# Performance work log

Hardware: AMD Instinct MI355X
Metric: run time of the kernel (lower is better)

Reference implementation:

```python
import jax, jax.numpy as jnp
import numpy as np

HEADS = 16

def setup_inputs() -> dict:
    key = jax.random.key(0)
    ks = jax.random.split(key, 6)
    b, n, d, k = 4, 4096, 1024, 256
    return {
        "x": jax.random.normal(ks[0], (b, n, d), dtype=jnp.float32),
        "Wq": jax.random.normal(ks[1], (d, d), dtype=jnp.float32) * 0.02,
        "Wk": jax.random.normal(ks[2], (d, d), dtype=jnp.float32) * 0.02,
        "Wv": jax.random.normal(ks[3], (d, d), dtype=jnp.float32) * 0.02,
        "proj_k": jax.random.normal(ks[4], (n, k), dtype=jnp.float32) * 0.02,
        "proj_v": jax.random.normal(ks[5], (n, k), dtype=jnp.float32) * 0.02,
    }

def reference(x, Wq, Wk, Wv, proj_k, proj_v):
    b, n, d = x.shape
    h = HEADS
    dh = d // h
    k = proj_k.shape[1]
    # Q/K/V projections (no bias)
    q = jnp.einsum('bnd,de->bne', x, Wq)          # [b,n,d]
    keys = jnp.einsum('bnd,de->bne', x, Wk)       # [b,n,d]
    vals = jnp.einsum('bnd,de->bne', x, Wv)       # [b,n,d]
    # low-rank sequence projection: n -> k
    keys = jnp.einsum('bnd,nk->bkd', keys, proj_k)   # [b,k,d]
    vals = jnp.einsum('bnd,nk->bkd', vals, proj_v)   # [b,k,d]
    # split heads
    q = q.reshape(b, n, h, dh).transpose(0, 2, 1, 3)      # [b,h,n,dh]
    keys = keys.reshape(b, k, h, dh).transpose(0, 2, 1, 3)  # [b,h,k,dh]
    vals = vals.reshape(b, k, h, dh).transpose(0, 2, 1, 3)  # [b,h,k,dh]
    # attention over reduced k dim (NOTE: module applies no 1/sqrt(dh) scale)
    dots = jnp.einsum('bhnd,bhkd->bhnk', q, keys)
    attn = jax.nn.softmax(dots, axis=-1)
    out = jnp.einsum('bhnk,bhkd->bhnd', attn, vals)
    return out.transpose(0, 2, 1, 3).reshape(b, n, d)
```

## Files before the change

### kernel.cpp

```cpp
#include <hip/hip_runtime.h>


typedef __fp16 f16x8 __attribute__((ext_vector_type(8)));
typedef __fp16 f16x2 __attribute__((ext_vector_type(2)));
typedef float fl4 __attribute__((ext_vector_type(4)));
typedef float f32x4 __attribute__((ext_vector_type(4)));
typedef unsigned int u32x2 __attribute__((ext_vector_type(2)));
typedef unsigned int u32x4 __attribute__((ext_vector_type(4)));

#define MFMA16(a, b, c) __builtin_amdgcn_mfma_f32_16x16x32_f16((a), (b), (c), 0, 0, 0)

__device__ __forceinline__ unsigned int pk2u(float a, float b) {
  f16x2 p = __builtin_amdgcn_cvt_pkrtz(a, b);
  return __builtin_bit_cast(unsigned int, p);
}

__device__ __forceinline__ f16x8 pk8(fl4 a, fl4 b) {
  f16x2 p0 = __builtin_amdgcn_cvt_pkrtz(a[0], a[1]);
  f16x2 p1 = __builtin_amdgcn_cvt_pkrtz(a[2], a[3]);
  f16x2 p2 = __builtin_amdgcn_cvt_pkrtz(b[0], b[1]);
  f16x2 p3 = __builtin_amdgcn_cvt_pkrtz(b[2], b[3]);
  f16x8 r;
  r[0] = p0[0]; r[1] = p0[1]; r[2] = p1[0]; r[3] = p1[1];
  r[4] = p2[0]; r[5] = p2[1]; r[6] = p3[0]; r[7] = p3[1];
  return r;
}

__device__ __forceinline__ void gload_lds16(const __fp16* g, void* lds_base) {
  __builtin_amdgcn_global_load_lds(
      (const __attribute__((address_space(1))) void*)g,
      (__attribute__((address_space(3))) void*)lds_base, 16, 0, 0);
}

__device__ __forceinline__ f16x8 rd128(const __fp16* base, int row, int ch) {
  return *(const f16x8*)((const char*)base + row * 128 +
                         ((ch ^ (row & 7)) * 16));
}

__device__ __forceinline__ void tr_cvt_body(
    float* tile, const float* in, __fp16* out, int R, int C, int bx, int by) {
  const int t = threadIdx.x;
  const int c0 = bx * 32, r0 = by * 32;
  {
    const int r = t >> 3, cg = (t & 7) * 4;
    fl4 v = *(const fl4*)(in + (size_t)(r0 + r) * C + c0 + cg);
    tile[r * 33 + cg] = v[0]; tile[r * 33 + cg + 1] = v[1];
    tile[r * 33 + cg + 2] = v[2]; tile[r * 33 + cg + 3] = v[3];
  }
  __syncthreads();
  {
    const int cc = t >> 3, rg = (t & 7) * 4;
    u32x2 p;
    p[0] = pk2u(tile[(rg + 0) * 33 + cc], tile[(rg + 1) * 33 + cc]);
    p[1] = pk2u(tile[(rg + 2) * 33 + cc], tile[(rg + 3) * 33 + cc]);
    *(u32x2*)(out + (size_t)(c0 + cc) * R + r0 + rg) = p;
  }
}

__global__ __launch_bounds__(256) void prep(
    const float* __restrict__ X, __fp16* __restrict__ Xf,
    __fp16* __restrict__ XT,
    const float* __restrict__ Wq, const float* __restrict__ Wk,
    const float* __restrict__ Wv, __fp16* __restrict__ WqT,
    __fp16* __restrict__ WkT, __fp16* __restrict__ WvT,
    const float* __restrict__ pk, const float* __restrict__ pv,
    __fp16* __restrict__ pkT, __fp16* __restrict__ pvT) {
  __shared__ float tile[32 * 65];
  const int id = blockIdx.x;
  const int t = threadIdx.x;
  if (id < 8192) {
    const int n0 = (id & 127) * 32, d0 = ((id >> 7) & 15) * 64, b = id >> 11;
    const float* src = X + ((size_t)b * 4096 + n0) * 1024 + d0;
    {
      const int r = t >> 3, cg = (t & 7) * 8;
      fl4 v0 = *(const fl4*)(src + (size_t)r * 1024 + cg);
      fl4 v1 = *(const fl4*)(src + (size_t)r * 1024 + cg + 4);
      *(f16x8*)(Xf + ((size_t)b * 4096 + n0 + r) * 1024 + d0 + cg) = pk8(v0, v1);
#pragma unroll
      for (int j = 0; j < 4; ++j) {
        tile[r * 65 + cg + j] = v0[j];
        tile[r * 65 + cg + 4 + j] = v1[j];
      }
    }
    __syncthreads();
    {
      const int d = t >> 2, ng = (t & 3) * 8;
      fl4 a, c;
#pragma unroll
      for (int j = 0; j < 4; ++j) {
        a[j] = tile[(ng + j) * 65 + d];
        c[j] = tile[(ng + 4 + j) * 65 + d];
      }
      *(f16x8*)(XT + ((size_t)b * 1024 + d0 + d) * 4096 + n0 + ng) = pk8(a, c);
    }
  } else if (id < 11264) {
    const int idx = id - 8192;
    const int z = idx >> 10;
    const float* in = (z == 0) ? Wq : (z == 1) ? Wk : Wv;
    __fp16* out = (z == 0) ? WqT : (z == 1) ? WkT : WvT;
    tr_cvt_body(tile, in, out, 1024, 1024, idx & 31, (idx >> 5) & 31);
  } else {
    const int idx = id - 11264;
    const int z = idx >> 10;
    tr_cvt_body(tile, z ? pv : pk, z ? pvT : pkT, 4096, 256, idx & 7,
                (idx >> 3) & 127);
  }
}

__global__ __launch_bounds__(256) void stage1_partial(
    const __fp16* __restrict__ pkT,
    const __fp16* __restrict__ pvT,
    const __fp16* __restrict__ XT,
    __fp16* __restrict__ Pk,
    __fp16* __restrict__ Pv) {
  __shared__ __fp16 Ak[64 * 64];
  __shared__ __fp16 Av[64 * 64];
  __shared__ __fp16 Bx[64 * 64];
  const int t = threadIdx.x;
  const int lane = t & 63, w = t >> 6;
  const int lr = lane & 15, lg = lane >> 4;
  const int fid = blockIdx.x;
  const int g = fid >> 5, s5 = fid & 31;
  const int kk0 = (s5 >> 3) * 64, p8 = s5 & 7;
  const int pr = g * 8 + p8;
  const int dd0 = (pr & 15) * 64;
  const int z = pr >> 4, b = z & 3, c = z >> 2;
  const int wr = (w >> 1) * 32, wc = (w & 1) * 32;

  f32x4 acck[2][2], accv[2][2];
#pragma unroll
  for (int i = 0; i < 2; ++i)
#pragma unroll
    for (int j = 0; j < 2; ++j) {
      acck[i][j] = (f32x4){0.f, 0.f, 0.f, 0.f};
      accv[i][j] = (f32x4){0.f, 0.f, 0.f, 0.f};
    }

  const int r8 = lane >> 3, c8 = lane & 7;
  const int ssw = ((c8 ^ r8) * 8);
  const __fp16* pkS0 = pkT + (size_t)(kk0 + w * 8 + r8) * 4096 + c * 1024 + ssw;
  const __fp16* pkS1 = pkS0 + (size_t)32 * 4096;
  const __fp16* pvS0 = pvT + (size_t)(kk0 + w * 8 + r8) * 4096 + c * 1024 + ssw;
  const __fp16* pvS1 = pvS0 + (size_t)32 * 4096;
  const __fp16* xS0 =
      XT + ((size_t)b * 1024 + dd0 + w * 8 + r8) * 4096 + c * 1024 + ssw;
  const __fp16* xS1 = xS0 + (size_t)32 * 4096;

  for (int it = 0; it < 16; ++it) {
    const int n0 = it * 64;
    __syncthreads();
    gload_lds16(pkS0 + n0, (char*)Ak + w * 1024);
    gload_lds16(pkS1 + n0, (char*)Ak + 4096 + w * 1024);
    gload_lds16(pvS0 + n0, (char*)Av + w * 1024);
    gload_lds16(pvS1 + n0, (char*)Av + 4096 + w * 1024);
    gload_lds16(xS0 + n0, (char*)Bx + w * 1024);
    gload_lds16(xS1 + n0, (char*)Bx + 4096 + w * 1024);
    __syncthreads();

#pragma unroll
    for (int s = 0; s < 2; ++s) {
      f16x8 ak[2], av[2], bx[2];
#pragma unroll
      for (int i = 0; i < 2; ++i) {
        ak[i] = rd128(Ak, wr + i * 16 + lr, s * 4 + lg);
        av[i] = rd128(Av, wr + i * 16 + lr, s * 4 + lg);
      }
#pragma unroll
      for (int j = 0; j < 2; ++j)
        bx[j] = rd128(Bx, wc + j * 16 + lr, s * 4 + lg);
#pragma unroll
      for (int i = 0; i < 2; ++i)
#pragma unroll
        for (int j = 0; j < 2; ++j) {
          acck[i][j] = MFMA16(ak[i], bx[j], acck[i][j]);
          accv[i][j] = MFMA16(av[i], bx[j], accv[i][j]);
        }
    }
  }

#pragma unroll
  for (int i = 0; i < 2; ++i)
#pragma unroll
    for (int j = 0; j < 2; ++j)
#pragma unroll
      for (int r = 0; r < 4; ++r) {
        const size_t row = (size_t)z * 256 + kk0 + wr + i * 16 + lg * 4 + r;
        const int col = dd0 + wc + j * 16 + lr;
        Pk[row * 1024 + col] = (__fp16)acck[i][j][r];
        Pv[row * 1024 + col] = (__fp16)accv[i][j][r];
      }
}

__global__ __launch_bounds__(256) void stage1_reduce(
    const __fp16* __restrict__ Pk, const __fp16* __restrict__ Pv,
    __fp16* __restrict__ Xk, __fp16* __restrict__ Xv) {
  const size_t idx = ((size_t)blockIdx.x * 256 + threadIdx.x) * 8;
  const int b = (int)(idx >> 18);
  const size_t rem = idx & 0x3FFFFu;
  float sk[8], sv[8];
#pragma unroll
  for (int j = 0; j < 8; ++j) { sk[j] = 0.f; sv[j] = 0.f; }
#pragma unroll
  for (int c = 0; c < 4; ++c) {
    const size_t off = (((size_t)(c * 4 + b)) << 18) + rem;
    f16x8 vk = *(const f16x8*)(Pk + off);
    f16x8 vv = *(const f16x8*)(Pv + off);
#pragma unroll
    for (int j = 0; j < 8; ++j) {
      sk[j] += (float)vk[j];
      sv[j] += (float)vv[j];
    }
  }
  f16x8 ok, ov;
#pragma unroll
  for (int j = 0; j < 8; ++j) {
    ok[j] = (__fp16)sk[j];
    ov[j] = (__fp16)sv[j];
  }
  *(f16x8*)(Xk + idx) = ok;
  *(f16x8*)(Xv + idx) = ov;
}

__global__ __launch_bounds__(256) void bt64z(
    const __fp16* __restrict__ Xk, const __fp16* __restrict__ WkT,
    __fp16* __restrict__ Kp, const __fp16* __restrict__ WvT,
    const __fp16* __restrict__ Xv, __fp16* __restrict__ Vpt) {
  constexpr int E = 1024;
  __shared__ __fp16 As[64 * 64];
  __shared__ __fp16 Bs[64 * 64];
  const int t = threadIdx.x;
  const int lane = t & 63, w = t >> 6;
  const int lr = lane & 15, lg = lane >> 4;
  int id = blockIdx.x;
  const __fp16 *A, *B;
  __fp16* C;
  int i0, j0, ldC;
  if (id < 256) {
    const int x = id & 3, y = (id >> 2) & 15, z = id >> 6;
    A = Xk + (size_t)z * 256 * 1024; B = WkT;
    C = Kp + (size_t)z * 256 * 1024;
    i0 = x * 64; j0 = y * 64; ldC = 1024;
  } else {
    id -= 256;
    const int x = id & 15, y = (id >> 4) & 3, z = id >> 6;
    A = WvT; B = Xv + (size_t)z * 256 * 1024;
    C = Vpt + (size_t)z * 1024 * 256;
    i0 = x * 64; j0 = y * 64; ldC = 256;
  }
  const int wr = (w >> 1) * 32, wc = (w & 1) * 32;

  f32x4 acc[2][2];
#pragma unroll
  for (int i = 0; i < 2; ++i)
#pragma unroll
    for (int j = 0; j < 2; ++j) acc[i][j] = (f32x4){0.f, 0.f, 0.f, 0.f};

  const int r8 = lane >> 3, c8 = lane & 7;
  const int ssw = ((c8 ^ r8) * 8);
  const __fp16* aS0 = A + (size_t)(i0 + w * 8 + r8) * E + ssw;
  const __fp16* aS1 = aS0 + (size_t)32 * E;
  const __fp16* bS0 = B + (size_t)(j0 + w * 8 + r8) * E + ssw;
  const __fp16* bS1 = bS0 + (size_t)32 * E;

  for (int it = 0; it < 16; ++it) {
    const int e0 = it * 64;
    __syncthreads();
    gload_lds16(aS0 + e0, (char*)As + w * 1024);
    gload_lds16(aS1 + e0, (char*)As + 4096 + w * 1024);
    gload_lds16(bS0 + e0, (char*)Bs + w * 1024);
    gload_lds16(bS1 + e0, (char*)Bs + 4096 + w * 1024);
    __syncthreads();

#pragma unroll
    for (int s = 0; s < 2; ++s) {
      f16x8 af[2], bf[2];
#pragma unroll
      for (int i = 0; i < 2; ++i)
        af[i] = rd128(As, wr + i * 16 + lr, s * 4 + lg);
#pragma unroll
      for (int j = 0; j < 2; ++j)
        bf[j] = rd128(Bs, wc + j * 16 + lr, s * 4 + lg);
#pragma unroll
      for (int i = 0; i < 2; ++i)
#pragma unroll
        for (int j = 0; j < 2; ++j)
          acc[i][j] = MFMA16(af[i], bf[j], acc[i][j]);
    }
  }

#pragma unroll
  for (int i = 0; i < 2; ++i)
#pragma unroll
    for (int j = 0; j < 2; ++j)
#pragma unroll
      for (int r = 0; r < 4; ++r) {
        const int row = i0 + wr + i * 16 + lg * 4 + r;
        const int col = j0 + wc + j * 16 + lr;
        C[(size_t)row * ldC + col] = (__fp16)acc[i][j][r];
      }
}

__global__ __launch_bounds__(512) void gemm_q(
    const __fp16* __restrict__ Xf,
    const __fp16* __restrict__ WT,
    __fp16* __restrict__ Q) {
  constexpr int K = 1024, N = 1024;
  __shared__ __fp16 Xs[256 * 64];
  __shared__ __fp16 Ws[128 * 64];
  const int t = threadIdx.x;
  const int lane = t & 63, w = t >> 6;
  const int lr = lane & 15, lg = lane >> 4;
  const int fid = blockIdx.x;
  const int m0 = (fid & 63) * 256;
  const int n0 = (fid >> 6) * 128;
  const int wr = (w & 3) * 64, wc = (w >> 2) * 64;

  f32x4 acc[4][4];
#pragma unroll
  for (int i = 0; i < 4; ++i)
#pragma unroll
    for (int j = 0; j < 4; ++j) acc[i][j] = (f32x4){0.f, 0.f, 0.f, 0.f};

  const int r8 = lane >> 3, c8 = lane & 7;
  const int ssw = ((c8 ^ r8) * 8);
  const __fp16* xS = Xf + (size_t)(m0 + w * 8 + r8) * K + ssw;
  const __fp16* wS = WT + (size_t)(n0 + w * 8 + r8) * K + ssw;

  for (int it = 0; it < 16; ++it) {
    const int k0 = it * 64;
    __syncthreads();
#pragma unroll
    for (int i = 0; i < 4; ++i)
      gload_lds16(xS + (size_t)i * 64 * K + k0, (char*)Xs + i * 8192 + w * 1024);
#pragma unroll
    for (int i = 0; i < 2; ++i)
      gload_lds16(wS + (size_t)i * 64 * K + k0, (char*)Ws + i * 8192 + w * 1024);
    __syncthreads();

#pragma unroll
    for (int s = 0; s < 2; ++s) {
      f16x8 af[4], bf[4];
#pragma unroll
      for (int i = 0; i < 4; ++i)
        af[i] = rd128(Xs, wr + i * 16 + lr, s * 4 + lg);
#pragma unroll
      for (int j = 0; j < 4; ++j)
        bf[j] = rd128(Ws, wc + j * 16 + lr, s * 4 + lg);
#pragma unroll
      for (int i = 0; i < 4; ++i)
#pragma unroll
        for (int j = 0; j < 4; ++j)
          acc[i][j] = MFMA16(af[i], bf[j], acc[i][j]);
    }
  }

#pragma unroll
  for (int i = 0; i < 4; ++i)
#pragma unroll
    for (int j = 0; j < 4; ++j)
#pragma unroll
      for (int r = 0; r < 4; ++r) {
        const int row = m0 + wr + i * 16 + lg * 4 + r;
        const int col = n0 + wc + j * 16 + lr;
        Q[(size_t)row * N + col] = (__fp16)acc[i][j][r];
      }
}

__global__ __launch_bounds__(256) void attn_k(
    const __fp16* __restrict__ Q,
    const __fp16* __restrict__ Kp,
    const __fp16* __restrict__ Vpt,
    float* __restrict__ O) {
  __shared__ __fp16 KV[256 * 64];
  const int t = threadIdx.x;
  const int lane = t & 63, w = t >> 6;
  const int lr = lane & 15, lg = lane >> 4;
  const int bh = blockIdx.x >> 5, rb = blockIdx.x & 31;
  const int b = bh >> 4, h = bh & 15;
  const int m0 = rb * 128 + w * 32;

  const __fp16* Kph = Kp + (size_t)b * 256 * 1024 + h * 64;
  const __fp16* Vph = Vpt + ((size_t)b * 1024 + h * 64) * 256;
  const __fp16* Qh = Q + ((size_t)(b * 4096 + m0)) * 1024 + h * 64;

#pragma unroll
  for (int i = 0; i < 8; ++i) {
    const int kr = (i * 4 + w) * 8 + (lane >> 3);
    gload_lds16(Kph + (size_t)kr * 1024 + (((lane & 7) ^ (kr & 7)) * 8),
                (char*)KV + (i * 4 + w) * 1024);
  }

  f16x8 aq[2][2];
#pragma unroll
  for (int mi = 0; mi < 2; ++mi)
#pragma unroll
    for (int s = 0; s < 2; ++s)
      aq[mi][s] =
          *(const f16x8*)(Qh + (size_t)(mi * 16 + lr) * 1024 + s * 32 + lg * 8);

  __syncthreads();

  f32x4 dots[2][16];
#pragma unroll
  for (int mi = 0; mi < 2; ++mi)
#pragma unroll
    for (int jt = 0; jt < 16; ++jt) dots[mi][jt] = (f32x4){0.f, 0.f, 0.f, 0.f};
#pragma unroll
  for (int jt = 0; jt < 16; ++jt) {
    const int r = jt * 16 + lr;
    f16x8 k0 = *(const f16x8*)((const char*)KV + r * 128 + ((lg ^ (r & 7)) * 16));
    f16x8 k1 =
        *(const f16x8*)((const char*)KV + r * 128 + (((4 + lg) ^ (r & 7)) * 16));
    dots[0][jt] = MFMA16(k0, aq[0][0], dots[0][jt]);
    dots[0][jt] = MFMA16(k1, aq[0][1], dots[0][jt]);
    dots[1][jt] = MFMA16(k0, aq[1][0], dots[1][jt]);
    dots[1][jt] = MFMA16(k1, aq[1][1], dots[1][jt]);
  }

  unsigned cpk[2][16][2];
  float smv[2];
#pragma unroll
  for (int mi = 0; mi < 2; ++mi) {
    float mx = -1e30f;
#pragma unroll
    for (int jt = 0; jt < 16; ++jt)
#pragma unroll
      for (int r = 0; r < 4; ++r) mx = fmaxf(mx, dots[mi][jt][r]);
    mx = fmaxf(mx, __shfl_xor(mx, 16, 64));
    mx = fmaxf(mx, __shfl_xor(mx, 32, 64));
    float sm = 0.f;
#pragma unroll
    for (int jt = 0; jt < 16; ++jt) {
#pragma unroll
      for (int r = 0; r < 4; ++r) {
        float p = __expf(dots[mi][jt][r] - mx);
        dots[mi][jt][r] = p;
        sm += p;
      }
      cpk[mi][jt][0] = pk2u(dots[mi][jt][0], dots[mi][jt][1]);
      cpk[mi][jt][1] = pk2u(dots[mi][jt][2], dots[mi][jt][3]);
    }
    sm += __shfl_xor(sm, 16, 64);
    sm += __shfl_xor(sm, 32, 64);
    smv[mi] = sm;
  }

  __syncthreads();

#pragma unroll
  for (int i = 0; i < 8; ++i) {
    const int dd = (i * 4 + w) * 2 + (lane >> 5);
    gload_lds16(Vph + (size_t)dd * 256 + (((lane & 31) ^ (dd & 7)) * 8),
                (char*)KV + (i * 4 + w) * 1024);
  }
  __syncthreads();

#pragma unroll
  for (int mi = 0; mi < 2; ++mi) {
    f32x4 o[4];
#pragma unroll
    for (int j = 0; j < 4; ++j) o[j] = (f32x4){0.f, 0.f, 0.f, 0.f};
#pragma unroll
    for (int ks = 0; ks < 8; ++ks) {
      u32x4 wds;
#pragma unroll
      for (int m = 0; m < 4; ++m) {
        const int addr = ((((lane & 16) >> 3) + (m >> 1)) * 16 + lr) * 4;
        const int a0 = __builtin_amdgcn_ds_bpermute(
            addr, (int)cpk[mi][ks * 2][m & 1]);
        const int a1 = __builtin_amdgcn_ds_bpermute(
            addr, (int)cpk[mi][ks * 2 + 1][m & 1]);
        wds[m] = (unsigned)((lg >> 1) ? a1 : a0);
      }
      f16x8 pa = __builtin_bit_cast(f16x8, wds);
#pragma unroll
      for (int jt2 = 0; jt2 < 4; ++jt2) {
        const int dd = jt2 * 16 + lr;
        f16x8 bv = *(const f16x8*)((const char*)KV + dd * 512 +
                                   (((ks * 4 + lg) ^ (dd & 7)) * 16));
        o[jt2] = MFMA16(pa, bv, o[jt2]);
      }
    }

    float rs[4];
#pragma unroll
    for (int r = 0; r < 4; ++r)
      rs[r] = 1.f / __shfl(smv[mi], (lane & 48) + lg * 4 + r, 64);
#pragma unroll
    for (int jt2 = 0; jt2 < 4; ++jt2)
#pragma unroll
      for (int r = 0; r < 4; ++r) {
        const size_t row = (size_t)(b * 4096 + m0 + mi * 16 + lg * 4 + r);
        O[row * 1024 + h * 64 + jt2 * 16 + lr] = o[jt2][r] * rs[r];
      }
  }
}

extern "C" void kernel_launch(void* const* d_in, const int* in_sizes, int n_in,
                              void* d_out, int out_size, void* d_ws, size_t ws_size,
                              hipStream_t stream) {
  (void)in_sizes; (void)n_in; (void)out_size; (void)ws_size;
  const float* x  = (const float*)d_in[0];
  const float* Wq = (const float*)d_in[1];
  const float* Wk = (const float*)d_in[2];
  const float* Wv = (const float*)d_in[3];
  const float* pk = (const float*)d_in[4];
  const float* pv = (const float*)d_in[5];
  float* out = (float*)d_out;

  __fp16* Qh  = (__fp16*)d_ws;
  __fp16* WqT = Qh  + (size_t)16384 * 1024;
  __fp16* WkT = WqT + (size_t)1024 * 1024;
  __fp16* WvT = WkT + (size_t)1024 * 1024;
  __fp16* pkT = WvT + (size_t)1024 * 1024;
  __fp16* pvT = pkT + (size_t)256 * 4096;
  __fp16* Xk  = pvT + (size_t)256 * 4096;
  __fp16* Xv  = Xk  + (size_t)4 * 256 * 1024;
  __fp16* Kp  = Xv  + (size_t)4 * 256 * 1024;
  __fp16* Vpt = Kp  + (size_t)4 * 256 * 1024;
  __fp16* Pk16 = (__fp16*)d_ws;
  __fp16* Pv16 = Pk16 + (size_t)16 * 256 * 1024;
  __fp16* Xf16 = (__fp16*)d_out;
  __fp16* XT   = Xf16 + (size_t)4 * 4096 * 1024;

  const dim3 bb(256);

  prep<<<dim3(13312), bb, 0, stream>>>(x, Xf16, XT, Wq, Wk, Wv, WqT, WkT, WvT,
                                       pk, pv, pkT, pvT);

  stage1_partial<<<dim3(1024), bb, 0, stream>>>(pkT, pvT, XT, Pk16, Pv16);
  stage1_reduce<<<dim3(512), bb, 0, stream>>>(Pk16, Pv16, Xk, Xv);

  bt64z<<<dim3(512), bb, 0, stream>>>(Xk, WkT, Kp, WvT, Xv, Vpt);

  gemm_q<<<dim3(512), dim3(512), 0, stream>>>(Xf16, WqT, Qh);

  attn_k<<<dim3(2048), bb, 0, stream>>>(Qh, Kp, Vpt, out);
}
```

Baseline: 155.8 us.

## Merge Q projection GEMM and stage1 partial into one launch

After: 157.6 us. No clear change (+1.2%).

```diff
diff --git a/kernel.cpp b/kernel.cpp
--- a/kernel.cpp
+++ b/kernel.cpp
@@ -189,6 +189,222 @@
         Pk[row * 1024 + col] = (__fp16)acck[i][j][r];
         Pv[row * 1024 + col] = (__fp16)accv[i][j][r];
       }
+}
+
+__global__ __launch_bounds__(512) void gemm_q(
+    const __fp16* __restrict__ Xf,
+    const __fp16* __restrict__ WT,
+    __fp16* __restrict__ Q) {
+  constexpr int K = 1024, N = 1024;
+  __shared__ __fp16 Xs[256 * 64];
+  __shared__ __fp16 Ws[128 * 64];
+  const int t = threadIdx.x;
+  const int lane = t & 63, w = t >> 6;
+  const int lr = lane & 15, lg = lane >> 4;
+  const int fid = blockIdx.x;
+  const int m0 = (fid & 63) * 256;
+  const int n0 = (fid >> 6) * 128;
+  const int wr = (w & 3) * 64, wc = (w >> 2) * 64;
+
+  f32x4 acc[4][4];
+#pragma unroll
+  for (int i = 0; i < 4; ++i)
+#pragma unroll
+    for (int j = 0; j < 4; ++j) acc[i][j] = (f32x4){0.f, 0.f, 0.f, 0.f};
+
+  const int r8 = lane >> 3, c8 = lane & 7;
+  const int ssw = ((c8 ^ r8) * 8);
+  const __fp16* xS = Xf + (size_t)(m0 + w * 8 + r8) * K + ssw;
+  const __fp16* wS = WT + (size_t)(n0 + w * 8 + r8) * K + ssw;
+
+  for (int it = 0; it < 16; ++it) {
+    const int k0 = it * 64;
+    __syncthreads();
+#pragma unroll
+    for (int i = 0; i < 4; ++i)
+      gload_lds16(xS + (size_t)i * 64 * K + k0, (char*)Xs + i * 8192 + w * 1024);
+#pragma unroll
+    for (int i = 0; i < 2; ++i)
+      gload_lds16(wS + (size_t)i * 64 * K + k0, (char*)Ws + i * 8192 + w * 1024);
+    __syncthreads();
+
+#pragma unroll
+    for (int s = 0; s < 2; ++s) {
+      f16x8 af[4], bf[4];
+#pragma unroll
+      for (int i = 0; i < 4; ++i)
+        af[i] = rd128(Xs, wr + i * 16 + lr, s * 4 + lg);
+#pragma unroll
+      for (int j = 0; j < 4; ++j)
+        bf[j] = rd128(Ws, wc + j * 16 + lr, s * 4 + lg);
+#pragma unroll
+      for (int i = 0; i < 4; ++i)
+#pragma unroll
+        for (int j = 0; j < 4; ++j)
+          acc[i][j] = MFMA16(af[i], bf[j], acc[i][j]);
+    }
+  }
+
+#pragma unroll
+  for (int i = 0; i < 4; ++i)
+#pragma unroll
+    for (int j = 0; j < 4; ++j)
+#pragma unroll
+      for (int r = 0; r < 4; ++r) {
+        const int row = m0 + wr + i * 16 + lg * 4 + r;
+        const int col = n0 + wc + j * 16 + lr;
+        Q[(size_t)row * N + col] = (__fp16)acc[i][j][r];
+      }
+}
+
+__global__ __launch_bounds__(512) void midphase(
+    const __fp16* __restrict__ Xf, const __fp16* __restrict__ WqT,
+    __fp16* __restrict__ Q,
+    const __fp16* __restrict__ pkT, const __fp16* __restrict__ pvT,
+    const __fp16* __restrict__ XT,
+    __fp16* __restrict__ Pk, __fp16* __restrict__ Pv) {
+  __shared__ __fp16 smem[24576];
+  const int id = blockIdx.x;
+  const int t = threadIdx.x;
+  const int lane = t & 63, w = t >> 6;
+  const int lr = lane & 15, lg = lane >> 4;
+  const int r8 = lane >> 3, c8 = lane & 7;
+  const int ssw = ((c8 ^ r8) * 8);
+
+  if (id < 512) {
+    constexpr int K = 1024, N = 1024;
+    __fp16* Xs = smem;
+    __fp16* Ws = smem + 16384;
+    const int m0 = (id & 63) * 256;
+    const int n0 = (id >> 6) * 128;
+    const int wr = (w & 3) * 64, wc = (w >> 2) * 64;
+
+    f32x4 acc[4][4];
+#pragma unroll
+    for (int i = 0; i < 4; ++i)
+#pragma unroll
+      for (int j = 0; j < 4; ++j) acc[i][j] = (f32x4){0.f, 0.f, 0.f, 0.f};
+
+    const __fp16* xS = Xf + (size_t)(m0 + w * 8 + r8) * K + ssw;
+    const __fp16* wS = WqT + (size_t)(n0 + w * 8 + r8) * K + ssw;
+
+    for (int it = 0; it < 16; ++it) {
+      const int k0 = it * 64;
+      __syncthreads();
+#pragma unroll
+      for (int i = 0; i < 4; ++i)
+        gload_lds16(xS + (size_t)i * 64 * K + k0, (char*)Xs + i * 8192 + w * 1024);
+#pragma unroll
+      for (int i = 0; i < 2; ++i)
+        gload_lds16(wS + (size_t)i * 64 * K + k0, (char*)Ws + i * 8192 + w * 1024);
+      __syncthreads();
+
+#pragma unroll
+      for (int s = 0; s < 2; ++s) {
+        f16x8 af[4], bf[4];
+#pragma unroll
+        for (int i = 0; i < 4; ++i)
+          af[i] = rd128(Xs, wr + i * 16 + lr, s * 4 + lg);
+#pragma unroll
+        for (int j = 0; j < 4; ++j)
+          bf[j] = rd128(Ws, wc + j * 16 + lr, s * 4 + lg);
+#pragma unroll
+        for (int i = 0; i < 4; ++i)
+#pragma unroll
+          for (int j = 0; j < 4; ++j)
+            acc[i][j] = MFMA16(af[i], bf[j], acc[i][j]);
+      }
+    }
+
+#pragma unroll
+    for (int i = 0; i < 4; ++i)
+#pragma unroll
+      for (int j = 0; j < 4; ++j)
+#pragma unroll
+        for (int r = 0; r < 4; ++r) {
+          const int row = m0 + wr + i * 16 + lg * 4 + r;
+          const int col = n0 + wc + j * 16 + lr;
+          Q[(size_t)row * N + col] = (__fp16)acc[i][j][r];
+        }
+  } else {
+    __fp16* Ak = smem;
+    __fp16* Av = smem + 4096;
+    __fp16* Bx = smem + 8192;
+    const int fid = id - 512;
+    const int g = fid >> 5, s5 = fid & 31;
+    const int kk0 = (s5 >> 3) * 64, p8 = s5 & 7;
+    const int pr = g * 8 + p8;
+    const int dd0 = (pr & 15) * 64;
+    const int z = pr >> 4, b = z & 3, c = z >> 2;
+    const int wr = (w >> 1) * 32, wc = (w & 1) * 32;
+
+    f32x4 acck[2][2], accv[2][2];
+#pragma unroll
+    for (int i = 0; i < 2; ++i)
+#pragma unroll
+      for (int j = 0; j < 2; ++j) {
+        acck[i][j] = (f32x4){0.f, 0.f, 0.f, 0.f};
+        accv[i][j] = (f32x4){0.f, 0.f, 0.f, 0.f};
+      }
+
+    const __fp16* pkS0 = pkT + (size_t)(kk0 + (w & 3) * 8 + r8) * 4096 + c * 1024 + ssw;
+    const __fp16* pkS1 = pkS0 + (size_t)32 * 4096;
+    const __fp16* pvS0 = pvT + (size_t)(kk0 + (w & 3) * 8 + r8) * 4096 + c * 1024 + ssw;
+    const __fp16* pvS1 = pvS0 + (size_t)32 * 4096;
+    const __fp16* xS0 =
+        XT + ((size_t)b * 1024 + dd0 + (w & 3) * 8 + r8) * 4096 + c * 1024 + ssw;
+    const __fp16* xS1 = xS0 + (size_t)32 * 4096;
+
+    for (int it = 0; it < 16; ++it) {
+      const int n0 = it * 64;
+      __syncthreads();
+      if (w < 4) {
+        gload_lds16(pkS0 + n0, (char*)Ak + w * 1024);
+        gload_lds16(pkS1 + n0, (char*)Ak + 4096 + w * 1024);
+        gload_lds16(pvS0 + n0, (char*)Av + w * 1024);
+        gload_lds16(pvS1 + n0, (char*)Av + 4096 + w * 1024);
+        gload_lds16(xS0 + n0, (char*)Bx + w * 1024);
+        gload_lds16(xS1 + n0, (char*)Bx + 4096 + w * 1024);
+      }
+      __syncthreads();
+
+      if (w < 4) {
+#pragma unroll
+        for (int s = 0; s < 2; ++s) {
+          f16x8 ak[2], av[2], bx[2];
+#pragma unroll
+          for (int i = 0; i < 2; ++i) {
+            ak[i] = rd128(Ak, wr + i * 16 + lr, s * 4 + lg);
+            av[i] = rd128(Av, wr + i * 16 + lr, s * 4 + lg);
+          }
+#pragma unroll
+          for (int j = 0; j < 2; ++j)
+            bx[j] = rd128(Bx, wc + j * 16 + lr, s * 4 + lg);
+#pragma unroll
+          for (int i = 0; i < 2; ++i)
+#pragma unroll
+            for (int j = 0; j < 2; ++j) {
+              acck[i][j] = MFMA16(ak[i], bx[j], acck[i][j]);
+              accv[i][j] = MFMA16(av[i], bx[j], accv[i][j]);
+            }
+        }
+      }
+    }
+
+    if (w < 4) {
+#pragma unroll
+      for (int i = 0; i < 2; ++i)
+#pragma unroll
+        for (int j = 0; j < 2; ++j)
+#pragma unroll
+          for (int r = 0; r < 4; ++r) {
+            const size_t row = (size_t)z * 256 + kk0 + wr + i * 16 + lg * 4 + r;
+            const int col = dd0 + wc + j * 16 + lr;
+            Pk[row * 1024 + col] = (__fp16)acck[i][j][r];
+            Pv[row * 1024 + col] = (__fp16)accv[i][j][r];
+          }
+    }
+  }
 }
 
 __global__ __launch_bounds__(256) void stage1_reduce(
@@ -300,72 +516,6 @@
       }
 }
 
-__global__ __launch_bounds__(512) void gemm_q(
-    const __fp16* __restrict__ Xf,
-    const __fp16* __restrict__ WT,
-    __fp16* __restrict__ Q) {
-  constexpr int K = 1024, N = 1024;
-  __shared__ __fp16 Xs[256 * 64];
-  __shared__ __fp16 Ws[128 * 64];
-  const int t = threadIdx.x;
-  const int lane = t & 63, w = t >> 6;
-  const int lr = lane & 15, lg = lane >> 4;
-  const int fid = blockIdx.x;
-  const int m0 = (fid & 63) * 256;
-  const int n0 = (fid >> 6) * 128;
-  const int wr = (w & 3) * 64, wc = (w >> 2) * 64;
-
-  f32x4 acc[4][4];
-#pragma unroll
-  for (int i = 0; i < 4; ++i)
-#pragma unroll
-    for (int j = 0; j < 4; ++j) acc[i][j] = (f32x4){0.f, 0.f, 0.f, 0.f};
-
-  const int r8 = lane >> 3, c8 = lane & 7;
-  const int ssw = ((c8 ^ r8) * 8);
-  const __fp16* xS = Xf + (size_t)(m0 + w * 8 + r8) * K + ssw;
-  const __fp16* wS = WT + (size_t)(n0 + w * 8 + r8) * K + ssw;
-
-  for (int it = 0; it < 16; ++it) {
-    const int k0 = it * 64;
-    __syncthreads();
-#pragma unroll
-    for (int i = 0; i < 4; ++i)
-      gload_lds16(xS + (size_t)i * 64 * K + k0, (char*)Xs + i * 8192 + w * 1024);
-#pragma unroll
-    for (int i = 0; i < 2; ++i)
-      gload_lds16(wS + (size_t)i * 64 * K + k0, (char*)Ws + i * 8192 + w * 1024);
-    __syncthreads();
-
-#pragma unroll
-    for (int s = 0; s < 2; ++s) {
-      f16x8 af[4], bf[4];
-#pragma unroll
-      for (int i = 0; i < 4; ++i)
-        af[i] = rd128(Xs, wr + i * 16 + lr, s * 4 + lg);
-#pragma unroll
-      for (int j = 0; j < 4; ++j)
-        bf[j] = rd128(Ws, wc + j * 16 + lr, s * 4 + lg);
-#pragma unroll
-      for (int i = 0; i < 4; ++i)
-#pragma unroll
-        for (int j = 0; j < 4; ++j)
-          acc[i][j] = MFMA16(af[i], bf[j], acc[i][j]);
-    }
-  }
-
-#pragma unroll
-  for (int i = 0; i < 4; ++i)
-#pragma unroll
-    for (int j = 0; j < 4; ++j)
-#pragma unroll
-      for (int r = 0; r < 4; ++r) {
-        const int row = m0 + wr + i * 16 + lg * 4 + r;
-        const int col = n0 + wc + j * 16 + lr;
-        Q[(size_t)row * N + col] = (__fp16)acc[i][j][r];
-      }
-}
-
 __global__ __launch_bounds__(256) void attn_k(
     const __fp16* __restrict__ Q,
     const __fp16* __restrict__ Kp,
@@ -499,7 +649,7 @@
 extern "C" void kernel_launch(void* const* d_in, const int* in_sizes, int n_in,
                               void* d_out, int out_size, void* d_ws, size_t ws_size,
                               hipStream_t stream) {
-  (void)in_sizes; (void)n_in; (void)out_size; (void)ws_size;
+  (void)in_sizes; (void)n_in; (void)out_size;
   const float* x  = (const float*)d_in[0];
   const float* Wq = (const float*)d_in[1];
   const float* Wk = (const float*)d_in[2];
@@ -518,22 +668,31 @@
   __fp16* Xv  = Xk  + (size_t)4 * 256 * 1024;
   __fp16* Kp  = Xv  + (size_t)4 * 256 * 1024;
   __fp16* Vpt = Kp  + (size_t)4 * 256 * 1024;
-  __fp16* Pk16 = (__fp16*)d_ws;
-  __fp16* Pv16 = Pk16 + (size_t)16 * 256 * 1024;
+  __fp16* wsEnd = Vpt + (size_t)4 * 256 * 1024;
   __fp16* Xf16 = (__fp16*)d_out;
   __fp16* XT   = Xf16 + (size_t)4 * 4096 * 1024;
 
+  const size_t needB = 52428800ULL + 2ULL * 16 * 256 * 1024 * 2;
+  const bool bigWs = (ws_size >= needB);
+  __fp16* Pk16 = bigWs ? wsEnd : (__fp16*)d_ws;
+  __fp16* Pv16 = Pk16 + (size_t)16 * 256 * 1024;
+
   const dim3 bb(256);
 
   prep<<<dim3(13312), bb, 0, stream>>>(x, Xf16, XT, Wq, Wk, Wv, WqT, WkT, WvT,
                                        pk, pv, pkT, pvT);
 
-  stage1_partial<<<dim3(1024), bb, 0, stream>>>(pkT, pvT, XT, Pk16, Pv16);
-  stage1_reduce<<<dim3(512), bb, 0, stream>>>(Pk16, Pv16, Xk, Xv);
-
-  bt64z<<<dim3(512), bb, 0, stream>>>(Xk, WkT, Kp, WvT, Xv, Vpt);
-
-  gemm_q<<<dim3(512), dim3(512), 0, stream>>>(Xf16, WqT, Qh);
+  if (bigWs) {
+    midphase<<<dim3(1536), dim3(512), 0, stream>>>(Xf16, WqT, Qh, pkT, pvT, XT,
+                                                   Pk16, Pv16);
+    stage1_reduce<<<dim3(512), bb, 0, stream>>>(Pk16, Pv16, Xk, Xv);
+    bt64z<<<dim3(512), bb, 0, stream>>>(Xk, WkT, Kp, WvT, Xv, Vpt);
+  } else {
+    stage1_partial<<<dim3(1024), bb, 0, stream>>>(pkT, pvT, XT, Pk16, Pv16);
+    stage1_reduce<<<dim3(512), bb, 0, stream>>>(Pk16, Pv16, Xk, Xv);
+    bt64z<<<dim3(512), bb, 0, stream>>>(Xk, WkT, Kp, WvT, Xv, Vpt);
+    gemm_q<<<dim3(512), dim3(512), 0, stream>>>(Xf16, WqT, Qh);
+  }
 
   attn_k<<<dim3(2048), bb, 0, stream>>>(Qh, Kp, Vpt, out);
 }
```

## Co-schedule Q projection GEMM with stage1 partial reduction in one launch

Applied to the files above, without the earlier changes.

After: 152.1 us, median of 2. 1.02x faster.

```diff
diff --git a/kernel.cpp b/kernel.cpp
--- a/kernel.cpp
+++ b/kernel.cpp
@@ -107,25 +107,18 @@
   }
 }
 
-__global__ __launch_bounds__(256) void stage1_partial(
-    const __fp16* __restrict__ pkT,
-    const __fp16* __restrict__ pvT,
-    const __fp16* __restrict__ XT,
-    __fp16* __restrict__ Pk,
-    __fp16* __restrict__ Pv) {
-  __shared__ __fp16 Ak[64 * 64];
-  __shared__ __fp16 Av[64 * 64];
-  __shared__ __fp16 Bx[64 * 64];
-  const int t = threadIdx.x;
-  const int lane = t & 63, w = t >> 6;
+__device__ __forceinline__ void stage1_tile(
+    const __fp16* __restrict__ pkT, const __fp16* __restrict__ pvT,
+    const __fp16* __restrict__ XT, __fp16* __restrict__ Pk,
+    __fp16* __restrict__ Pv, __fp16* Ak, __fp16* Av, __fp16* Bx,
+    int fid, int ww, int lane) {
   const int lr = lane & 15, lg = lane >> 4;
-  const int fid = blockIdx.x;
   const int g = fid >> 5, s5 = fid & 31;
   const int kk0 = (s5 >> 3) * 64, p8 = s5 & 7;
   const int pr = g * 8 + p8;
   const int dd0 = (pr & 15) * 64;
   const int z = pr >> 4, b = z & 3, c = z >> 2;
-  const int wr = (w >> 1) * 32, wc = (w & 1) * 32;
+  const int wr = (ww >> 1) * 32, wc = (ww & 1) * 32;
 
   f32x4 acck[2][2], accv[2][2];
 #pragma unroll
@@ -138,23 +131,23 @@
 
   const int r8 = lane >> 3, c8 = lane & 7;
   const int ssw = ((c8 ^ r8) * 8);
-  const __fp16* pkS0 = pkT + (size_t)(kk0 + w * 8 + r8) * 4096 + c * 1024 + ssw;
+  const __fp16* pkS0 = pkT + (size_t)(kk0 + ww * 8 + r8) * 4096 + c * 1024 + ssw;
   const __fp16* pkS1 = pkS0 + (size_t)32 * 4096;
-  const __fp16* pvS0 = pvT + (size_t)(kk0 + w * 8 + r8) * 4096 + c * 1024 + ssw;
+  const __fp16* pvS0 = pvT + (size_t)(kk0 + ww * 8 + r8) * 4096 + c * 1024 + ssw;
   const __fp16* pvS1 = pvS0 + (size_t)32 * 4096;
   const __fp16* xS0 =
-      XT + ((size_t)b * 1024 + dd0 + w * 8 + r8) * 4096 + c * 1024 + ssw;
+      XT + ((size_t)b * 1024 + dd0 + ww * 8 + r8) * 4096 + c * 1024 + ssw;
   const __fp16* xS1 = xS0 + (size_t)32 * 4096;
 
   for (int it = 0; it < 16; ++it) {
     const int n0 = it * 64;
     __syncthreads();
-    gload_lds16(pkS0 + n0, (char*)Ak + w * 1024);
-    gload_lds16(pkS1 + n0, (char*)Ak + 4096 + w * 1024);
-    gload_lds16(pvS0 + n0, (char*)Av + w * 1024);
-    gload_lds16(pvS1 + n0, (char*)Av + 4096 + w * 1024);
-    gload_lds16(xS0 + n0, (char*)Bx + w * 1024);
-    gload_lds16(xS1 + n0, (char*)Bx + 4096 + w * 1024);
+    gload_lds16(pkS0 + n0, (char*)Ak + ww * 1024);
+    gload_lds16(pkS1 + n0, (char*)Ak + 4096 + ww * 1024);
+    gload_lds16(pvS0 + n0, (char*)Av + ww * 1024);
+    gload_lds16(pvS1 + n0, (char*)Av + 4096 + ww * 1024);
+    gload_lds16(xS0 + n0, (char*)Bx + ww * 1024);
+    gload_lds16(xS1 + n0, (char*)Bx + 4096 + ww * 1024);
     __syncthreads();
 
 #pragma unroll
@@ -189,6 +182,106 @@
         Pk[row * 1024 + col] = (__fp16)acck[i][j][r];
         Pv[row * 1024 + col] = (__fp16)accv[i][j][r];
       }
+}
+
+__global__ __launch_bounds__(256) void stage1_partial(
+    const __fp16* __restrict__ pkT, const __fp16* __restrict__ pvT,
+    const __fp16* __restrict__ XT, __fp16* __restrict__ Pk,
+    __fp16* __restrict__ Pv) {
+  __shared__ __fp16 smem[12288];
+  const int t = threadIdx.x;
+  stage1_tile(pkT, pvT, XT, Pk, Pv, smem, smem + 4096, smem + 8192,
+              blockIdx.x, t >> 6, t & 63);
+}
+
+__device__ __forceinline__ void gemmq_tile(
+    const __fp16* __restrict__ Xf, const __fp16* __restrict__ WT,
+    __fp16* __restrict__ Q, __fp16* Xs, __fp16* Ws, int fid, int w,
+    int lane) {
+  constexpr int K = 1024, N = 1024;
+  const int lr = lane & 15, lg = lane >> 4;
+  const int m0 = (fid & 63) * 256;
+  const int n0 = (fid >> 6) * 128;
+  const int wr = (w & 3) * 64, wc = (w >> 2) * 64;
+
+  f32x4 acc[4][4];
+#pragma unroll
+  for (int i = 0; i < 4; ++i)
+#pragma unroll
+    for (int j = 0; j < 4; ++j) acc[i][j] = (f32x4){0.f, 0.f, 0.f, 0.f};
+
+  const int r8 = lane >> 3, c8 = lane & 7;
+  const int ssw = ((c8 ^ r8) * 8);
+  const __fp16* xS = Xf + (size_t)(m0 + w * 8 + r8) * K + ssw;
+  const __fp16* wS = WT + (size_t)(n0 + w * 8 + r8) * K + ssw;
+
+  for (int it = 0; it < 16; ++it) {
+    const int k0 = it * 64;
+    __syncthreads();
+#pragma unroll
+    for (int i = 0; i < 4; ++i)
+      gload_lds16(xS + (size_t)i * 64 * K + k0, (char*)Xs + i * 8192 + w * 1024);
+#pragma unroll
+    for (int i = 0; i < 2; ++i)
+      gload_lds16(wS + (size_t)i * 64 * K + k0, (char*)Ws + i * 8192 + w * 1024);
+    __syncthreads();
+
+#pragma unroll
+    for (int s = 0; s < 2; ++s) {
+      f16x8 af[4], bf[4];
+#pragma unroll
+      for (int i = 0; i < 4; ++i)
+        af[i] = rd128(Xs, wr + i * 16 + lr, s * 4 + lg);
+#pragma unroll
+      for (int j = 0; j < 4; ++j)
+        bf[j] = rd128(Ws, wc + j * 16 + lr, s * 4 + lg);
+#pragma unroll
+      for (int i = 0; i < 4; ++i)
+#pragma unroll
+        for (int j = 0; j < 4; ++j)
+          acc[i][j] = MFMA16(af[i], bf[j], acc[i][j]);
+    }
+  }
+
+#pragma unroll
+  for (int i = 0; i < 4; ++i)
+#pragma unroll
+    for (int j = 0; j < 4; ++j)
+#pragma unroll
+      for (int r = 0; r < 4; ++r) {
+        const int row = m0 + wr + i * 16 + lg * 4 + r;
+        const int col = n0 + wc + j * 16 + lr;
+        Q[(size_t)row * N + col] = (__fp16)acc[i][j][r];
+      }
+}
+
+__global__ __launch_bounds__(512) void gemm_q(
+    const __fp16* __restrict__ Xf, const __fp16* __restrict__ WT,
+    __fp16* __restrict__ Q) {
+  __shared__ __fp16 smem[24576];
+  const int t = threadIdx.x;
+  gemmq_tile(Xf, WT, Q, smem, smem + 16384, blockIdx.x, t >> 6, t & 63);
+}
+
+__global__ __launch_bounds__(512) void midphase(
+    const __fp16* __restrict__ Xf, const __fp16* __restrict__ WqT,
+    __fp16* __restrict__ Q,
+    const __fp16* __restrict__ pkT, const __fp16* __restrict__ pvT,
+    const __fp16* __restrict__ XT,
+    __fp16* __restrict__ Pk, __fp16* __restrict__ Pv) {
+  __shared__ __fp16 smem[24576];
+  const int id = blockIdx.x;
+  const int t = threadIdx.x;
+  const int lane = t & 63, w = t >> 6;
+
+  if (id < 512) {
+    gemmq_tile(Xf, WqT, Q, smem, smem + 16384, id, w, lane);
+  } else {
+    const int grp = w >> 2, ww = w & 3;
+    __fp16* base = smem + grp * 12288;
+    stage1_tile(pkT, pvT, XT, Pk, Pv, base, base + 4096, base + 8192,
+                (id - 512) * 2 + grp, ww, lane);
+  }
 }
 
 __global__ __launch_bounds__(256) void stage1_reduce(
@@ -300,72 +393,6 @@
       }
 }
 
-__global__ __launch_bounds__(512) void gemm_q(
-    const __fp16* __restrict__ Xf,
-    const __fp16* __restrict__ WT,
-    __fp16* __restrict__ Q) {
-  constexpr int K = 1024, N = 1024;
-  __shared__ __fp16 Xs[256 * 64];
-  __shared__ __fp16 Ws[128 * 64];
-  const int t = threadIdx.x;
-  const int lane = t & 63, w = t >> 6;
-  const int lr = lane & 15, lg = lane >> 4;
-  const int fid = blockIdx.x;
-  const int m0 = (fid & 63) * 256;
-  const int n0 = (fid >> 6) * 128;
-  const int wr = (w & 3) * 64, wc = (w >> 2) * 64;
-
-  f32x4 acc[4][4];
-#pragma unroll
-  for (int i = 0; i < 4; ++i)
-#pragma unroll
-    for (int j = 0; j < 4; ++j) acc[i][j] = (f32x4){0.f, 0.f, 0.f, 0.f};
-
-  const int r8 = lane >> 3, c8 = lane & 7;
-  const int ssw = ((c8 ^ r8) * 8);
-  const __fp16* xS = Xf + (size_t)(m0 + w * 8 + r8) * K + ssw;
-  const __fp16* wS = WT + (size_t)(n0 + w * 8 + r8) * K + ssw;
-
-  for (int it = 0; it < 16; ++it) {
-    const int k0 = it * 64;
-    __syncthreads();
-#pragma unroll
-    for (int i = 0; i < 4; ++i)
-      gload_lds16(xS + (size_t)i * 64 * K + k0, (char*)Xs + i * 8192 + w * 1024);
-#pragma unroll
-    for (int i = 0; i < 2; ++i)
-      gload_lds16(wS + (size_t)i * 64 * K + k0, (char*)Ws + i * 8192 + w * 1024);
-    __syncthreads();
-
-#pragma unroll
-    for (int s = 0; s < 2; ++s) {
-      f16x8 af[4], bf[4];
-#pragma unroll
-      for (int i = 0; i < 4; ++i)
-        af[i] = rd128(Xs, wr + i * 16 + lr, s * 4 + lg);
-#pragma unroll
-      for (int j = 0; j < 4; ++j)
-        bf[j] = rd128(Ws, wc + j * 16 + lr, s * 4 + lg);
-#pragma unroll
-      for (int i = 0; i < 4; ++i)
-#pragma unroll
-        for (int j = 0; j < 4; ++j)
-          acc[i][j] = MFMA16(af[i], bf[j], acc[i][j]);
-    }
-  }
-
-#pragma unroll
-  for (int i = 0; i < 4; ++i)
-#pragma unroll
-    for (int j = 0; j < 4; ++j)
-#pragma unroll
-      for (int r = 0; r < 4; ++r) {
-        const int row = m0 + wr + i * 16 + lg * 4 + r;
-        const int col = n0 + wc + j * 16 + lr;
-        Q[(size_t)row * N + col] = (__fp16)acc[i][j][r];
-      }
-}
-
 __global__ __launch_bounds__(256) void attn_k(
     const __fp16* __restrict__ Q,
     const __fp16* __restrict__ Kp,
@@ -499,7 +526,7 @@
 extern "C" void kernel_launch(void* const* d_in, const int* in_sizes, int n_in,
                               void* d_out, int out_size, void* d_ws, size_t ws_size,
                               hipStream_t stream) {
-  (void)in_sizes; (void)n_in; (void)out_size; (void)ws_size;
+  (void)in_sizes; (void)n_in; (void)out_size;
   const float* x  = (const float*)d_in[0];
   const float* Wq = (const float*)d_in[1];
   const float* Wk = (const float*)d_in[2];
@@ -518,22 +545,31 @@
   __fp16* Xv  = Xk  + (size_t)4 * 256 * 1024;
   __fp16* Kp  = Xv  + (size_t)4 * 256 * 1024;
   __fp16* Vpt = Kp  + (size_t)4 * 256 * 1024;
-  __fp16* Pk16 = (__fp16*)d_ws;
-  __fp16* Pv16 = Pk16 + (size_t)16 * 256 * 1024;
+  __fp16* wsEnd = Vpt + (size_t)4 * 256 * 1024;
   __fp16* Xf16 = (__fp16*)d_out;
   __fp16* XT   = Xf16 + (size_t)4 * 4096 * 1024;
 
+  const size_t needB = 52428800ULL + 2ULL * 16 * 256 * 1024 * 2;
+  const bool bigWs = (ws_size >= needB);
+  __fp16* Pk16 = bigWs ? wsEnd : (__fp16*)d_ws;
+  __fp16* Pv16 = Pk16 + (size_t)16 * 256 * 1024;
+
   const dim3 bb(256);
 
   prep<<<dim3(13312), bb, 0, stream>>>(x, Xf16, XT, Wq, Wk, Wv, WqT, WkT, WvT,
                                        pk, pv, pkT, pvT);
 
-  stage1_partial<<<dim3(1024), bb, 0, stream>>>(pkT, pvT, XT, Pk16, Pv16);
-  stage1_reduce<<<dim3(512), bb, 0, stream>>>(Pk16, Pv16, Xk, Xv);
-
-  bt64z<<<dim3(512), bb, 0, stream>>>(Xk, WkT, Kp, WvT, Xv, Vpt);
-
-  gemm_q<<<dim3(512), dim3(512), 0, stream>>>(Xf16, WqT, Qh);
+  if (bigWs) {
+    midphase<<<dim3(1024), dim3(512), 0, stream>>>(Xf16, WqT, Qh, pkT, pvT, XT,
+                                                   Pk16, Pv16);
+    stage1_reduce<<<dim3(512), bb, 0, stream>>>(Pk16, Pv16, Xk, Xv);
+    bt64z<<<dim3(512), bb, 0, stream>>>(Xk, WkT, Kp, WvT, Xv, Vpt);
+  } else {
+    stage1_partial<<<dim3(1024), bb, 0, stream>>>(pkT, pvT, XT, Pk16, Pv16);
+    stage1_reduce<<<dim3(512), bb, 0, stream>>>(Pk16, Pv16, Xk, Xv);
+    bt64z<<<dim3(512), bb, 0, stream>>>(Xk, WkT, Kp, WvT, Xv, Vpt);
+    gemm_q<<<dim3(512), dim3(512), 0, stream>>>(Xf16, WqT, Qh);
+  }
 
   attn_k<<<dim3(2048), bb, 0, stream>>>(Qh, Kp, Vpt, out);
 }
```
